# Kernel optimization log

Measured on AMD Instinct MI355X. Metric: run time of the kernel, lower is better.

The kernel has to match this reference:

```python
import jax, jax.numpy as jnp
import numpy as np

DEPTH = 4
CH = 3
SIG_CHANNELS = 3 + 9 + 27 + 81  # signatory.signature_channels(3, 4) = 120


def _tp(a, b):
    # flattened tensor (outer) product: (N, p) x (N, q) -> (N, p*q), row-major (signatory ordering)
    return (a[:, :, None] * b[:, None, :]).reshape(a.shape[0], -1)


def _signature(path):
    """Depth-4 path signature of path: (N, T, 3) -> (N, 120).

    Segment signature of a linear piece with increment dx is exp(dx):
    levels dx^{otimes k} / k!. Segments are combined with Chen's identity
    via a lax.scan over the time axis.
    """
    dx = path[:, 1:, :] - path[:, :-1, :]  # (N, T-1, 3)
    N, Tm1, _ = dx.shape
    dt = path.dtype
    # per-segment signature levels (flattened)
    s1 = dx                                                                # (N,T-1,3)
    s2 = (s1[..., :, None] * dx[..., None, :]).reshape(N, Tm1, 9) / 2.0   # dx^2/2!
    s3 = (s2[..., :, None] * dx[..., None, :]).reshape(N, Tm1, 27) / 3.0  # dx^3/3!
    s4 = (s3[..., :, None] * dx[..., None, :]).reshape(N, Tm1, 81) / 4.0  # dx^4/4!
    segs = (jnp.moveaxis(s1, 1, 0), jnp.moveaxis(s2, 1, 0),
            jnp.moveaxis(s3, 1, 0), jnp.moveaxis(s4, 1, 0))  # time-leading for scan

    init = (jnp.zeros((N, 3), dt), jnp.zeros((N, 9), dt),
            jnp.zeros((N, 27), dt), jnp.zeros((N, 81), dt))

    def chen_step(carry, seg):
        c1, c2, c3, c4 = carry
        g1, g2, g3, g4 = seg
        n1 = c1 + g1
        n2 = c2 + _tp(c1, g1) + g2
        n3 = c3 + _tp(c2, g1) + _tp(c1, g2) + g3
        n4 = c4 + _tp(c3, g1) + _tp(c2, g2) + _tp(c1, g3) + g4
        return (n1, n2, n3, n4), None

    (c1, c2, c3, c4), _ = jax.lax.scan(chen_step, init, segs)
    return jnp.concatenate([c1, c2, c3, c4], axis=1)  # (N, 120)


def setup_inputs() -> dict:
    key = jax.random.key(0)
    k1, k2, k3, k4, k5 = jax.random.split(key, 5)
    B, T, V, M = 64, 300, 17, 2
    inp = jax.random.normal(k1, (B, CH, T, V, M), dtype=jnp.float32)
    fan1 = 34 * SIG_CHANNELS  # 4080
    W1 = jax.random.uniform(k2, (512, fan1), jnp.float32, -1.0, 1.0) / np.sqrt(fan1)
    b1 = jax.random.uniform(k3, (512,), jnp.float32, -1.0, 1.0) / np.sqrt(fan1)
    W2 = jax.random.uniform(k4, (155, 512), jnp.float32, -1.0, 1.0) / np.sqrt(512)
    b2 = jax.random.uniform(k5, (155,), jnp.float32, -1.0, 1.0) / np.sqrt(512)
    return {"inp": inp, "W1": W1, "b1": b1, "W2": W2, "b2": b2}


def reference(inp, W1, b1, W2, b2):
    B, _, T, V, M = inp.shape
    # order matches the torch loop: for v in range(17): for m in range(2)
    paths = jnp.transpose(inp, (0, 3, 4, 2, 1)).reshape(B * V * M, T, CH)  # (B*34, T, 3)
    sig = _signature(paths).reshape(B, V * M * SIG_CHANNELS)  # (B, 4080)
    h = sig @ W1.T + b1  # dropout is identity in eval mode
    return h @ W2.T + b2  # (B, 155)
```

## Files before the change

### kernel.cpp

```cpp
#include <hip/hip_runtime.h>
#include <hip/hip_bf16.h>

#define B_SZ 64
#define T_PTS 300
#define N_SEG 299
#define VM 34
#define NPATH (B_SZ*VM)
#define SIGC 120
#define FAN1 4080
#define H1 512
#define NOUT 155
#define CHUNK 5
#define TT 75
#define KSPL 48
#define KW 85
#define JPW 8

__device__ __forceinline__ void sig_append(float a1[3], float a2[9], float a3[27], float a4[81],
                                           float d0, float d1, float d2) {
  const float d[3] = {d0, d1, d2};

  float Z[3], Y[9], X[27];
#pragma unroll
  for (int i = 0; i < 3; i++) Z[i] = fmaf(d[i], 1.0f / 24.0f, (1.0f / 6.0f) * a1[i]);
#pragma unroll
  for (int e = 0; e < 9; e++) Y[e] = fmaf(d[e % 3], Z[e / 3], 0.5f * a2[e]);
#pragma unroll
  for (int e = 0; e < 27; e++) X[e] = fmaf(d[e % 3], Y[e / 3], a3[e]);
#pragma unroll
  for (int e = 0; e < 81; e++) a4[e] = fmaf(d[e % 3], X[e / 3], a4[e]);

  float Z3[3], Y3[9];
#pragma unroll
  for (int i = 0; i < 3; i++) Z3[i] = fmaf(d[i], 1.0f / 6.0f, 0.5f * a1[i]);
#pragma unroll
  for (int e = 0; e < 9; e++) Y3[e] = fmaf(d[e % 3], Z3[e / 3], a2[e]);
#pragma unroll
  for (int e = 0; e < 27; e++) a3[e] = fmaf(d[e % 3], Y3[e / 3], a3[e]);

  float Z2[3];
#pragma unroll
  for (int i = 0; i < 3; i++) Z2[i] = fmaf(d[i], 0.5f, a1[i]);
#pragma unroll
  for (int e = 0; e < 9; e++) a2[e] = fmaf(d[e % 3], Z2[e / 3], a2[e]);

#pragma unroll
  for (int i = 0; i < 3; i++) a1[i] += d[i];
}

template <int OFF>
__device__ __forceinline__ float lane_down(float x) {
  if constexpr (OFF < 16) {
    return __int_as_float(__builtin_amdgcn_update_dpp(
        0, __float_as_int(x), 0x100 + OFF , 0xF, 0xF, true));
  } else {
    return __shfl_xor(x, OFF);
  }
}

template <int OFF>
__device__ __forceinline__ void chen_round(float a1[3], float a2[9], float a3[27], float a4[81]) {
  float B1[3], B2[9], B3[27];
#pragma unroll
  for (int i = 0; i < 3; i++) B1[i] = lane_down<OFF>(a1[i]);
#pragma unroll
  for (int i = 0; i < 9; i++) B2[i] = lane_down<OFF>(a2[i]);
#pragma unroll
  for (int i = 0; i < 27; i++) B3[i] = lane_down<OFF>(a3[i]);

#pragma unroll
  for (int e = 0; e < 81; e++) {
    const float b4 = lane_down<OFF>(a4[e]);
    float v = a4[e] + b4;
    v = fmaf(a3[e / 3], B1[e % 3], v);
    v = fmaf(a2[e / 9], B2[e % 9], v);
    v = fmaf(a1[e / 27], B3[e % 27], v);
    a4[e] = v;
  }
#pragma unroll
  for (int e = 0; e < 27; e++) {
    float v = a3[e] + B3[e];
    v = fmaf(a2[e / 3], B1[e % 3], v);
    v = fmaf(a1[e / 9], B2[e % 9], v);
    a3[e] = v;
  }
#pragma unroll
  for (int e = 0; e < 9; e++) a2[e] = fmaf(a1[e / 3], B1[e % 3], a2[e] + B2[e]);
#pragma unroll
  for (int i = 0; i < 3; i++) a1[i] += B1[i];
}

__global__ __launch_bounds__(256) void transpose_kernel(const float* __restrict__ inp,
                                                        float* __restrict__ tp,
                                                        const float* __restrict__ b1,
                                                        float* __restrict__ ht) {
  const int b = blockIdx.x;
  const int tile = blockIdx.y;
  const int t0 = tile * TT;
  const int tid = threadIdx.x;
  __shared__ float lds[3 * TT * VM];

  const float* src = inp + (size_t)b * 3 * T_PTS * VM;
  for (int idx = tid; idx < 3 * TT * VM; idx += 256) {
    const int c = idx / (TT * VM);
    const int rem = idx - c * (TT * VM);
    lds[idx] = src[(c * T_PTS + t0) * VM + rem];
  }
  __syncthreads();

  for (int idx = tid; idx < VM * TT * 3; idx += 256) {
    const int vm = idx / (TT * 3);
    const int i = idx - vm * (TT * 3);
    const int tt = i / 3;
    const int c = i - tt * 3;
    tp[((size_t)(b * VM + vm) * T_PTS + t0 + tt) * 3 + c] = lds[(c * TT + tt) * VM + vm];
  }

  if (tile == 0) {
    for (int idx = tid; idx < 8 * 64; idx += 256)
      ht[(size_t)(8 * b) * 64 + idx] = b1[8 * b + (idx >> 6)];
  }
}

__global__ __launch_bounds__(64)
__attribute__((amdgpu_waves_per_eu(1)))
void sig_kernel(const float* __restrict__ tp, float* __restrict__ St) {
  const int lane = threadIdx.x & 63;
  const int p = blockIdx.x;
  const int t0 = lane * CHUNK;

  const float* bp = tp + (size_t)p * (T_PTS * 3) + t0 * 3;

  float a1[3], a2[9], a3[27], a4[81];
#pragma unroll
  for (int i = 0; i < 3; i++) a1[i] = 0.f;
#pragma unroll
  for (int i = 0; i < 9; i++) a2[i] = 0.f;
#pragma unroll
  for (int i = 0; i < 27; i++) a3[i] = 0.f;
#pragma unroll
  for (int i = 0; i < 81; i++) a4[i] = 0.f;

  float x0 = bp[0], x1 = bp[1], x2 = bp[2];
#pragma unroll
  for (int s = 0; s < CHUNK; s++) {
    const float y0 = bp[3 * s + 3];
    const float y1 = bp[3 * s + 4];
    const float y2 = bp[3 * s + 5];
    const bool valid = (t0 + s) < N_SEG;
    const float d0 = valid ? (y0 - x0) : 0.0f;
    const float d1 = valid ? (y1 - x1) : 0.0f;
    const float d2 = valid ? (y2 - x2) : 0.0f;
    sig_append(a1, a2, a3, a4, d0, d1, d2);
    x0 = y0; x1 = y1; x2 = y2;
  }

  chen_round<1>(a1, a2, a3, a4);
  chen_round<2>(a1, a2, a3, a4);
  chen_round<4>(a1, a2, a3, a4);
  chen_round<8>(a1, a2, a3, a4);
  chen_round<16>(a1, a2, a3, a4);
  chen_round<32>(a1, a2, a3, a4);

  if (lane == 0) {
    const int b = p / VM;
    const int vm = p - b * VM;
    float* dst = St + (size_t)(vm * SIGC) * 64 + b;
#pragma unroll
    for (int i = 0; i < 3; i++) dst[(size_t)i * 64] = a1[i];
#pragma unroll
    for (int i = 0; i < 9; i++) dst[(size_t)(3 + i) * 64] = a2[i];
#pragma unroll
    for (int i = 0; i < 27; i++) dst[(size_t)(12 + i) * 64] = a3[i];
#pragma unroll
    for (int i = 0; i < 81; i++) dst[(size_t)(39 + i) * 64] = a4[i];
  }
}

__global__ __launch_bounds__(256) void gemm1_kernel(const float* __restrict__ St,
                                                    const float* __restrict__ W1,
                                                    float* __restrict__ ht) {
  const int lane = threadIdx.x & 63;
  int wave_id = (blockIdx.x * 256 + threadIdx.x) >> 6;
  wave_id = __builtin_amdgcn_readfirstlane(wave_id);
  const int ks = wave_id >> 6;
  const int jg = wave_id & 63;
  const int k0 = ks * KW;

  const float* stp = St + (size_t)k0 * 64 + lane;
  const float* w[JPW];
#pragma unroll
  for (int r = 0; r < JPW; r++) w[r] = W1 + (size_t)(jg * JPW + r) * FAN1 + k0;

  float sv[KW];
#pragma unroll
  for (int i = 0; i < KW; i++) sv[i] = stp[(size_t)i * 64];

  float acc[JPW];
#pragma unroll
  for (int r = 0; r < JPW; r++) acc[r] = 0.f;

#pragma unroll
  for (int i = 0; i < KW; i++) {
#pragma unroll
    for (int r = 0; r < JPW; r++) acc[r] = fmaf(sv[i], w[r][i], acc[r]);
  }

  float* hp = ht + (size_t)(jg * JPW) * 64 + lane;
#pragma unroll
  for (int r = 0; r < JPW; r++) atomicAdd(hp + r * 64, acc[r]);
}

__global__ __launch_bounds__(256) void gemm2_kernel(const float* __restrict__ ht,
                                                    const float* __restrict__ W2,
                                                    const float* __restrict__ b2,
                                                    float* __restrict__ out) {
  const int j = blockIdx.x;
  const int lane = threadIdx.x & 63;
  int w = threadIdx.x >> 6;
  w = __builtin_amdgcn_readfirstlane(w);
  __shared__ float red[4][64];

  const float* htp = ht + (size_t)(w * 128) * 64 + lane;
  const float* w2r = W2 + (size_t)j * H1 + w * 128;
  float acc = 0.f;
#pragma unroll 8
  for (int k = 0; k < 128; k++) acc = fmaf(w2r[k], htp[(size_t)k * 64], acc);

  red[w][lane] = acc;
  __syncthreads();
  if (threadIdx.x < 64) {
    const float tot = red[0][lane] + red[1][lane] + red[2][lane] + red[3][lane];
    out[(size_t)lane * NOUT + j] = tot + b2[j];
  }
}

extern "C" void kernel_launch(void* const* d_in, const int* in_sizes, int n_in,
                              void* d_out, int out_size, void* d_ws, size_t ws_size,
                              hipStream_t stream) {
  const float* inp = (const float*)d_in[0];
  const float* W1  = (const float*)d_in[1];
  const float* b1  = (const float*)d_in[2];
  const float* W2  = (const float*)d_in[3];
  const float* b2  = (const float*)d_in[4];
  float* out = (float*)d_out;

  float* tpbuf = (float*)d_ws;
  float* St    = tpbuf + (size_t)NPATH * T_PTS * 3;
  float* ht    = St + (size_t)FAN1 * 64;

  transpose_kernel<<<dim3(B_SZ, 4), 256, 0, stream>>>(inp, tpbuf, b1, ht);
  sig_kernel<<<NPATH, 64, 0, stream>>>(tpbuf, St);
  gemm1_kernel<<<KSPL * 64 / 4, 256, 0, stream>>>(St, W1, ht);
  gemm2_kernel<<<NOUT, 256, 0, stream>>>(ht, W2, b2, out);
}
```

Before: 117.6 us.

## Drop transpose kernel; read strided input directly in signature kernel, fold b1 into gemm2

Removes the separate transpose pass, so the signature kernel gathers path points directly from the original (B,C,T,V,M) layout with a stride of VM floats. The hidden-buffer bias initialisation moves into the signature kernel as zero-fill, and b1 is instead applied in gemm2 by accumulating W2·b1 alongside the main dot product. This saves one launch and a round trip of the transposed buffer through memory. In exchange, the per-lane loads become uncoalesced strided gathers, and gemm2 does a small amount of extra work.

```diff
diff --git a/kernel.cpp b/kernel.cpp
--- a/kernel.cpp
+++ b/kernel.cpp
@@ -11,7 +11,6 @@
 #define H1 512
 #define NOUT 155
 #define CHUNK 5
-#define TT 75
 #define KSPL 48
 #define KW 85
 #define JPW 8
@@ -90,46 +89,26 @@
   for (int i = 0; i < 3; i++) a1[i] += B1[i];
 }
 
-__global__ __launch_bounds__(256) void transpose_kernel(const float* __restrict__ inp,
-                                                        float* __restrict__ tp,
-                                                        const float* __restrict__ b1,
-                                                        float* __restrict__ ht) {
-  const int b = blockIdx.x;
-  const int tile = blockIdx.y;
-  const int t0 = tile * TT;
-  const int tid = threadIdx.x;
-  __shared__ float lds[3 * TT * VM];
-
-  const float* src = inp + (size_t)b * 3 * T_PTS * VM;
-  for (int idx = tid; idx < 3 * TT * VM; idx += 256) {
-    const int c = idx / (TT * VM);
-    const int rem = idx - c * (TT * VM);
-    lds[idx] = src[(c * T_PTS + t0) * VM + rem];
-  }
-  __syncthreads();
-
-  for (int idx = tid; idx < VM * TT * 3; idx += 256) {
-    const int vm = idx / (TT * 3);
-    const int i = idx - vm * (TT * 3);
-    const int tt = i / 3;
-    const int c = i - tt * 3;
-    tp[((size_t)(b * VM + vm) * T_PTS + t0 + tt) * 3 + c] = lds[(c * TT + tt) * VM + vm];
-  }
-
-  if (tile == 0) {
-    for (int idx = tid; idx < 8 * 64; idx += 256)
-      ht[(size_t)(8 * b) * 64 + idx] = b1[8 * b + (idx >> 6)];
-  }
-}
-
 __global__ __launch_bounds__(64)
 __attribute__((amdgpu_waves_per_eu(1)))
-void sig_kernel(const float* __restrict__ tp, float* __restrict__ St) {
+void sig_kernel(const float* __restrict__ inp, float* __restrict__ St,
+                float* __restrict__ ht) {
   const int lane = threadIdx.x & 63;
   const int p = blockIdx.x;
+  if (p < H1) ht[(size_t)p * 64 + lane] = 0.0f;
+
+  const int b = p / VM;
+  const int vm = p - b * VM;
   const int t0 = lane * CHUNK;
 
-  const float* bp = tp + (size_t)p * (T_PTS * 3) + t0 * 3;
+  const float* base = inp + (size_t)b * 3 * T_PTS * VM + vm;
+
+  int tv[CHUNK + 1];
+#pragma unroll
+  for (int s = 0; s <= CHUNK; s++) {
+    const int t = t0 + s;
+    tv[s] = t < N_SEG ? t : N_SEG;
+  }
 
   float a1[3], a2[9], a3[27], a4[81];
 #pragma unroll
@@ -141,12 +120,14 @@
 #pragma unroll
   for (int i = 0; i < 81; i++) a4[i] = 0.f;
 
-  float x0 = bp[0], x1 = bp[1], x2 = bp[2];
+  float x0 = base[0 * T_PTS * VM + tv[0] * VM];
+  float x1 = base[1 * T_PTS * VM + tv[0] * VM];
+  float x2 = base[2 * T_PTS * VM + tv[0] * VM];
 #pragma unroll
   for (int s = 0; s < CHUNK; s++) {
-    const float y0 = bp[3 * s + 3];
-    const float y1 = bp[3 * s + 4];
-    const float y2 = bp[3 * s + 5];
+    const float y0 = base[0 * T_PTS * VM + tv[s + 1] * VM];
+    const float y1 = base[1 * T_PTS * VM + tv[s + 1] * VM];
+    const float y2 = base[2 * T_PTS * VM + tv[s + 1] * VM];
     const bool valid = (t0 + s) < N_SEG;
     const float d0 = valid ? (y0 - x0) : 0.0f;
     const float d1 = valid ? (y1 - x1) : 0.0f;
@@ -163,8 +144,6 @@
   chen_round<32>(a1, a2, a3, a4);
 
   if (lane == 0) {
-    const int b = p / VM;
-    const int vm = p - b * VM;
     float* dst = St + (size_t)(vm * SIGC) * 64 + b;
 #pragma unroll
     for (int i = 0; i < 3; i++) dst[(size_t)i * 64] = a1[i];
@@ -213,6 +192,7 @@
 
 __global__ __launch_bounds__(256) void gemm2_kernel(const float* __restrict__ ht,
                                                     const float* __restrict__ W2,
+                                                    const float* __restrict__ b1,
                                                     const float* __restrict__ b2,
                                                     float* __restrict__ out) {
   const int j = blockIdx.x;
@@ -223,11 +203,16 @@
 
   const float* htp = ht + (size_t)(w * 128) * 64 + lane;
   const float* w2r = W2 + (size_t)j * H1 + w * 128;
-  float acc = 0.f;
+  const float* b1r = b1 + w * 128;
+  float acc = 0.f, accb = 0.f;
 #pragma unroll 8
-  for (int k = 0; k < 128; k++) acc = fmaf(w2r[k], htp[(size_t)k * 64], acc);
-
-  red[w][lane] = acc;
+  for (int k = 0; k < 128; k++) {
+    const float wv = w2r[k];
+    acc = fmaf(wv, htp[(size_t)k * 64], acc);
+    accb = fmaf(wv, b1r[k], accb);
+  }
+
+  red[w][lane] = acc + accb;
   __syncthreads();
   if (threadIdx.x < 64) {
     const float tot = red[0][lane] + red[1][lane] + red[2][lane] + red[3][lane];
@@ -245,12 +230,10 @@
   const float* b2  = (const float*)d_in[4];
   float* out = (float*)d_out;
 
-  float* tpbuf = (float*)d_ws;
-  float* St    = tpbuf + (size_t)NPATH * T_PTS * 3;
-  float* ht    = St + (size_t)FAN1 * 64;
-
-  transpose_kernel<<<dim3(B_SZ, 4), 256, 0, stream>>>(inp, tpbuf, b1, ht);
-  sig_kernel<<<NPATH, 64, 0, stream>>>(tpbuf, St);
+  float* St = (float*)d_ws;
+  float* ht = St + (size_t)FAN1 * 64;
+
+  sig_kernel<<<NPATH, 64, 0, stream>>>(inp, St, ht);
   gemm1_kernel<<<KSPL * 64 / 4, 256, 0, stream>>>(St, W1, ht);
-  gemm2_kernel<<<NOUT, 256, 0, stream>>>(ht, W2, b2, out);
-}
+  gemm2_kernel<<<NOUT, 256, 0, stream>>>(ht, W2, b1, b2, out);
+}
```

Result: faster. 114.2 us (-2.9%).
